# Kernel optimization log

Hardware: AMD Instinct MI355X
Metric: run time of the kernel (lower is better)

The kernel has to match this reference:

```python
import jax, jax.numpy as jnp
import numpy as np

EPS = 1e-5

def _layernorm(h):
    # parameter-free LayerNorm over last dim (elementwise_affine=False)
    mu = jnp.mean(h, axis=-1, keepdims=True)
    var = jnp.mean(jnp.square(h - mu), axis=-1, keepdims=True)
    return (h - mu) / jnp.sqrt(var + EPS)

def setup_inputs() -> dict:
    key = jax.random.key(0)
    k1, k2, k3, k4 = jax.random.split(key, 4)
    B, D, F_, I = 16, 37, 4096, 64
    x = jax.random.normal(k1, (B, D, F_), dtype=jnp.float32)
    s = 1.0 / np.sqrt(D)  # ~ torch Linear default init scale
    Wq = jax.random.normal(k2, (D, I), dtype=jnp.float32) * s
    Wk = jax.random.normal(k3, (D, I), dtype=jnp.float32) * s
    Wv = jax.random.normal(k4, (D, I), dtype=jnp.float32) * s
    return {"x": x, "Wq": Wq, "Wk": Wk, "Wv": Wv}

def reference(x, Wq, Wk, Wv):
    # x: [B, depth, featuresize] -> entities [B, F, depth]
    xb = jnp.transpose(x, (0, 2, 1))
    q = _layernorm(jnp.einsum('bfd,di->bfi', xb, Wq))
    k = _layernorm(jnp.einsum('bfd,di->bfi', xb, Wk))
    v = _layernorm(jnp.einsum('bfd,di->bfi', xb, Wv))
    d = q.shape[-1]
    att = jnp.einsum('bqi,bki->bqk', q, k) / jnp.sqrt(jnp.float32(d))
    # faithful to torch: softmax over dim=1 (the query axis), not the key axis
    weights = jax.nn.softmax(att, axis=-2)
    return jnp.einsum('bqk,bki->bqi', weights, v)
```

## Files before the change

### kernel.cpp

```cpp
#include <hip/hip_runtime.h>
#include <math.h>

#define B_  16
#define D_  37
#define F_  4096
#define I_  64
#define EPS 1e-5f
#define QSCALE 0.18033688011112042f
#define NQS 2

typedef unsigned short u16;
typedef __bf16 bf16x8 __attribute__((ext_vector_type(8)));
typedef __bf16 bf16x2v __attribute__((ext_vector_type(2)));
typedef float  f32x16 __attribute__((ext_vector_type(16)));
typedef float  f32x2v __attribute__((ext_vector_type(2)));
typedef unsigned int u32x4 __attribute__((ext_vector_type(4)));
typedef int i32x2 __attribute__((ext_vector_type(2)));

#define ZERO16 {0,0,0,0, 0,0,0,0, 0,0,0,0, 0,0,0,0}
#define MFMA32(a, b, c) __builtin_amdgcn_mfma_f32_32x32x16_bf16((a), (b), (c), 0, 0, 0)

#if __has_builtin(__builtin_amdgcn_exp2f)
#define EX2(x) __builtin_amdgcn_exp2f(x)
#else
#define EX2(x) exp2f(x)
#endif
#if __has_builtin(__builtin_amdgcn_rcpf)
#define RCP(x) __builtin_amdgcn_rcpf(x)
#else
#define RCP(x) (1.f / (x))
#endif

__device__ __forceinline__ u16 f2b(float f) {
  unsigned u = __builtin_bit_cast(unsigned, f);
  return (u16)((u + 0x7fffu + ((u >> 16) & 1u)) >> 16);
}
__device__ __forceinline__ unsigned pk2(float lo, float hi) {
  f32x2v f = {lo, hi};
  bf16x2v h = __builtin_convertvector(f, bf16x2v);
  return __builtin_bit_cast(unsigned, h);
}

__device__ __forceinline__ void plswap(unsigned& a, unsigned& b) {
#if __has_builtin(__builtin_amdgcn_permlane32_swap)
  i32x2 r = __builtin_amdgcn_permlane32_swap((int)a, (int)b, false, false);
  a = (unsigned)r[0];
  b = (unsigned)r[1];
#else
  const int lh = (int)((threadIdx.x & 63) >> 5);
  unsigned pa = (unsigned)__shfl_xor((int)a, 32, 64);
  unsigned pb = (unsigned)__shfl_xor((int)b, 32, 64);
  unsigned na = lh ? pb : a;
  unsigned nb = lh ? b : pa;
  a = na;
  b = nb;
#endif
}

__device__ __forceinline__ void build_af(const f32x16& s, bf16x8& f0, bf16x8& f1) {
  float e[16];
#pragma unroll
  for (int r = 0; r < 16; ++r) e[r] = EX2(s[r]);
  unsigned a = pk2(e[0], e[1]),   bq = pk2(e[2], e[3]);
  unsigned c = pk2(e[4], e[5]),   d  = pk2(e[6], e[7]);
  plswap(a, c);
  plswap(bq, d);
  u32x4 v0 = {a, bq, c, d};
  f0 = __builtin_bit_cast(bf16x8, v0);
  unsigned ee = pk2(e[8], e[9]),  ff = pk2(e[10], e[11]);
  unsigned g  = pk2(e[12], e[13]), h = pk2(e[14], e[15]);
  plswap(ee, g);
  plswap(ff, h);
  u32x4 v1 = {ee, ff, g, h};
  f1 = __builtin_bit_cast(bf16x8, v1);
}

__device__ __forceinline__ bf16x8 ldfrag(const u16* base, int row, int kb) {
  return *(const bf16x8*)(base + (row << 6) + ((kb ^ (row & 7)) << 3));
}
__device__ __forceinline__ void stage16(u16* dst, const u16* src, int c, int spitch) {
  const int r = c >> 3, cb = c & 7;
  const int4 v = *(const int4*)(src + (size_t)r * spitch + (cb << 3));
  *(int4*)(dst + (r << 6) + ((cb ^ (r & 7)) << 3)) = v;
}
__device__ __forceinline__ int soff_l(int c) {
  const int r = c >> 3, cb = c & 7;
  return (r << 6) + ((cb ^ (r & 7)) << 3);
}
__device__ __forceinline__ int soff_g(int c, int spitch) {
  return (c >> 3) * spitch + ((c & 7) << 3);
}

__global__ __launch_bounds__(256) void qkv_ln_k(
    const float* __restrict__ x,
    const float* __restrict__ Wq, const float* __restrict__ Wk,
    const float* __restrict__ Wv,
    u16* __restrict__ qn, u16* __restrict__ kn, u16* __restrict__ vt) {
  __shared__ float sW[3 * D_ * I_];
  __shared__ float xs[D_ * 64];
  __shared__ __align__(16) u16 vtile[64 * 72];

  const int t = threadIdx.x;
  const int b = blockIdx.y;
  const int f0 = blockIdx.x * 64;

  for (int i = t; i < D_ * I_; i += 256) {
    sW[i]               = Wq[i];
    sW[D_ * I_ + i]     = Wk[i];
    sW[2 * D_ * I_ + i] = Wv[i];
  }
  const float* xb = x + (size_t)b * D_ * F_ + f0;
  for (int i = t; i < D_ * 64; i += 256)
    xs[i] = xb[(size_t)(i >> 6) * F_ + (i & 63)];
  __syncthreads();

  const int lane = t & 63, w = t >> 6;

  for (int it = 0; it < 16; ++it) {
    const int fl = w * 16 + it;
    float hq = 0.f, hk = 0.f, hv = 0.f;
#pragma unroll
    for (int d = 0; d < D_; ++d) {
      const float xv = xs[d * 64 + fl];
      hq = fmaf(xv, sW[d * 64 + lane], hq);
      hk = fmaf(xv, sW[D_ * I_ + d * 64 + lane], hk);
      hv = fmaf(xv, sW[2 * D_ * I_ + d * 64 + lane], hv);
    }
    auto lnorm = [&](float a) -> float {
      float s = a;
#pragma unroll
      for (int o = 32; o > 0; o >>= 1) s += __shfl_xor(s, o, 64);
      const float mu = s * (1.f / 64.f);
      const float d0 = a - mu;
      float v = d0 * d0;
#pragma unroll
      for (int o = 32; o > 0; o >>= 1) v += __shfl_xor(v, o, 64);
      return d0 * rsqrtf(v * (1.f / 64.f) + EPS);
    };
    const size_t fo = ((size_t)b * F_ + f0 + fl) * I_ + lane;
    qn[fo] = f2b(lnorm(hq) * QSCALE);
    kn[fo] = f2b(lnorm(hk));
    vtile[lane * 72 + fl] = f2b(lnorm(hv));
  }
  __syncthreads();
  for (int p = 0; p < 2; ++p) {
    const int c = p * 256 + t;
    const int r = c >> 3, off = (c & 7) * 8;
    const int4 v = *(const int4*)&vtile[r * 72 + off];
    *(int4*)(vt + ((size_t)b * I_ + r) * F_ + f0 + off) = v;
  }
}

__global__ __launch_bounds__(256, 2) void attn_stats_k(
    const u16* __restrict__ qn, const u16* __restrict__ kn,
    float* __restrict__ zp) {
  __shared__ __align__(16) u16 sm[16384];

  const int t = threadIdx.x, lane = t & 63, w = t >> 6;
  const int l31 = lane & 31, lh = lane >> 5;
  const int b = blockIdx.y, k0 = blockIdx.x * 256, qh = blockIdx.z;

  const u16* kb = kn + ((size_t)b * F_ + k0) * I_;
#pragma unroll
  for (int p = 0; p < 8; ++p) stage16(sm, kb, p * 256 + t, 64);
  __syncthreads();
  bf16x8 kf[2][4];
#pragma unroll
  for (int kb2 = 0; kb2 < 2; ++kb2)
#pragma unroll
    for (int ic = 0; ic < 4; ++ic)
      kf[kb2][ic] = ldfrag(sm + (w * 64 + kb2 * 32) * 64, l31, ic * 2 + lh);
  __syncthreads();

  int qoff_l[2], qoff_g[2];
#pragma unroll
  for (int p = 0; p < 2; ++p) {
    const int c = p * 256 + t;
    qoff_l[p] = soff_l(c);
    qoff_g[p] = soff_g(c, 64);
  }

  const u16* qsrc = qn + ((size_t)b * F_ + qh * (F_ / NQS)) * I_;
#pragma unroll
  for (int p = 0; p < 2; ++p)
    *(int4*)(sm + qoff_l[p]) = *(const int4*)(qsrc + qoff_g[p]);
  qsrc += 64 * I_;

  float Zc[2][2] = {{0.f, 0.f}, {0.f, 0.f}};
  const int NC = F_ / NQS / 64;

  for (int c = 0; c < NC; ++c) {
    const int cur = (c & 1) * 4096;
    __syncthreads();
    if (c + 1 < NC) {
      const int nxt = cur ^ 4096;
#pragma unroll
      for (int p = 0; p < 2; ++p)
        *(int4*)(sm + nxt + qoff_l[p]) = *(const int4*)(qsrc + qoff_g[p]);
      qsrc += 64 * I_;
    }

    f32x16 a00 = ZERO16, a01 = ZERO16, a10 = ZERO16, a11 = ZERO16;
#pragma unroll
    for (int ic = 0; ic < 4; ++ic) {
      const bf16x8 q0f = ldfrag(sm + cur, l31, ic * 2 + lh);
      const bf16x8 q1f = ldfrag(sm + cur + 32 * 64, l31, ic * 2 + lh);
      a00 = MFMA32(q0f, kf[0][ic], a00);
      a01 = MFMA32(q0f, kf[1][ic], a01);
      a10 = MFMA32(q1f, kf[0][ic], a10);
      a11 = MFMA32(q1f, kf[1][ic], a11);
    }
#pragma unroll
    for (int r = 0; r < 16; ++r) {
      Zc[0][0] += EX2(a00[r]);
      Zc[0][1] += EX2(a01[r]);
      Zc[1][0] += EX2(a10[r]);
      Zc[1][1] += EX2(a11[r]);
    }
  }

#pragma unroll
  for (int kb2 = 0; kb2 < 2; ++kb2) {
    float Zt = Zc[0][kb2] + Zc[1][kb2];
    Zt += __shfl_xor(Zt, 32, 64);
    if (lane < 32)
      zp[((size_t)qh * B_ + b) * F_ + k0 + w * 64 + kb2 * 32 + lane] = Zt;
  }
}

__global__ __launch_bounds__(256) void vscale_k(u16* __restrict__ vt,
                                                const float* __restrict__ zp) {
  const int b = blockIdx.y;
  const int off = (blockIdx.x * 256 + (int)threadIdx.x) * 8;
  const int k = off & (F_ - 1);
  u16* p = vt + (size_t)b * I_ * F_ + off;
  const float* z0 = zp + (size_t)b * F_ + k;
  const float* z1 = zp + (size_t)B_ * F_ + (size_t)b * F_ + k;
  int4 raw = *(const int4*)p;
  u16 es[8], os[8];
  *(int4*)es = raw;
#pragma unroll
  for (int j = 0; j < 8; ++j) {
    const float v = __builtin_bit_cast(float, (unsigned)es[j] << 16);
    const float rz = RCP(z0[j] + z1[j]);
    os[j] = f2b(v * rz);
  }
  *(int4*)p = *(int4*)os;
}

__global__ __launch_bounds__(128, 2) void attn_out_k(
    const u16* __restrict__ qn, const u16* __restrict__ kn,
    const u16* __restrict__ vt, float* __restrict__ out) {
  __shared__ __align__(16) u16 sm[16384];

  const int t = threadIdx.x, lane = t & 63, w = t >> 6;
  const int l31 = lane & 31, lh = lane >> 5;
  const int b = blockIdx.y, q0 = blockIdx.x * 128;

  const u16* qb = qn + ((size_t)b * F_ + q0) * I_;
#pragma unroll
  for (int p = 0; p < 8; ++p) stage16(sm, qb, p * 128 + t, 64);
  __syncthreads();
  bf16x8 qf[2][4];
#pragma unroll
  for (int qb2 = 0; qb2 < 2; ++qb2)
#pragma unroll
    for (int ic = 0; ic < 4; ++ic)
      qf[qb2][ic] = ldfrag(sm + (w * 64 + qb2 * 32) * 64, l31, ic * 2 + lh);
  __syncthreads();

  int off_l[4], kg[4], vg[4];
#pragma unroll
  for (int p = 0; p < 4; ++p) {
    const int c = p * 128 + t;
    off_l[p] = soff_l(c);
    kg[p] = soff_g(c, 64);
    vg[p] = soff_g(c, F_);
  }

  const u16* ksrc = kn + (size_t)b * F_ * I_;
  const u16* vsrc = vt + (size_t)b * I_ * F_;
#pragma unroll
  for (int p = 0; p < 4; ++p) {
    *(int4*)(sm + off_l[p])        = *(const int4*)(ksrc + kg[p]);
    *(int4*)(sm + 8192 + off_l[p]) = *(const int4*)(vsrc + vg[p]);
  }
  ksrc += 64 * I_;
  vsrc += 64;

  f32x16 o00 = ZERO16, o01 = ZERO16, o10 = ZERO16, o11 = ZERO16;
  const int NC = F_ / 64;

  for (int c = 0; c < NC; ++c) {
    const int cur = (c & 1) * 4096;
    __syncthreads();
    if (c + 1 < NC) {
      const int nxt = cur ^ 4096;
#pragma unroll
      for (int p = 0; p < 4; ++p) {
        *(int4*)(sm + nxt + off_l[p])        = *(const int4*)(ksrc + kg[p]);
        *(int4*)(sm + 8192 + nxt + off_l[p]) = *(const int4*)(vsrc + vg[p]);
      }
      ksrc += 64 * I_;
      vsrc += 64;
    }

    const u16* Kc = sm + cur;
    f32x16 s00 = ZERO16, s01 = ZERO16, s10 = ZERO16, s11 = ZERO16;
#pragma unroll
    for (int ic = 0; ic < 4; ++ic) {
      const bf16x8 ak0 = ldfrag(Kc, l31, ic * 2 + lh);
      const bf16x8 ak1 = ldfrag(Kc + 32 * 64, l31, ic * 2 + lh);
      s00 = MFMA32(ak0, qf[0][ic], s00);
      s01 = MFMA32(ak0, qf[1][ic], s01);
      s10 = MFMA32(ak1, qf[0][ic], s10);
      s11 = MFMA32(ak1, qf[1][ic], s11);
    }

    bf16x8 af[2][4];
    build_af(s00, af[0][0], af[0][1]);
    build_af(s10, af[0][2], af[0][3]);
    build_af(s01, af[1][0], af[1][1]);
    build_af(s11, af[1][2], af[1][3]);

    const u16* Vc = sm + 8192 + cur;
#pragma unroll
    for (int kb4 = 0; kb4 < 4; ++kb4) {
      const bf16x8 bv0 = ldfrag(Vc, l31, kb4 * 2 + lh);
      const bf16x8 bv1 = ldfrag(Vc + 32 * 64, l31, kb4 * 2 + lh);
      o00 = MFMA32(af[0][kb4], bv0, o00);
      o01 = MFMA32(af[0][kb4], bv1, o01);
      o10 = MFMA32(af[1][kb4], bv0, o10);
      o11 = MFMA32(af[1][kb4], bv1, o11);
    }
  }

  float* ob = out + ((size_t)b * F_ + q0 + w * 64) * I_;
#pragma unroll
  for (int r = 0; r < 16; ++r) {
    const int qr = (r & 3) + 8 * (r >> 2) + 4 * lh;
    ob[(size_t)qr * I_ + l31]              = o00[r];
    ob[(size_t)qr * I_ + 32 + l31]         = o01[r];
    ob[(size_t)(32 + qr) * I_ + l31]       = o10[r];
    ob[(size_t)(32 + qr) * I_ + 32 + l31]  = o11[r];
  }
}

extern "C" void kernel_launch(void* const* d_in, const int* in_sizes, int n_in,
                              void* d_out, int out_size, void* d_ws,
                              size_t ws_size, hipStream_t stream) {
  const float* x  = (const float*)d_in[0];
  const float* Wq = (const float*)d_in[1];
  const float* Wk = (const float*)d_in[2];
  const float* Wv = (const float*)d_in[3];
  float* out = (float*)d_out;

  const size_t NBF = (size_t)B_ * F_ * I_;
  u16* qn   = (u16*)d_ws;
  u16* kn   = qn + NBF;
  u16* vt   = kn + NBF;
  float* zp = (float*)(vt + NBF);

  qkv_ln_k<<<dim3(F_ / 64, B_), 256, 0, stream>>>(x, Wq, Wk, Wv, qn, kn, vt);
  attn_stats_k<<<dim3(F_ / 256, B_, NQS), 256, 0, stream>>>(qn, kn, zp);
  vscale_k<<<dim3(I_ * F_ / 2048, B_), 256, 0, stream>>>(vt, zp);
  attn_out_k<<<dim3(F_ / 128, B_), 128, 0, stream>>>(qn, kn, vt, out);
}
```

Baseline: 273.5 us.

## Split attention output over key chunks with atomics and register-block QKV projection

The output kernel now splits the key axis four ways across a new grid dimension. Each block processes 32-key chunks with half the shared memory, and partial outputs are accumulated into the zeroed result with atomicAdd. The stats kernel doubles its query split and raises its occupancy hint, and vscale sums all partial Z values. The QKV projection drops its shared-memory staging and keeps 16 rows per wave in registers, reading x and weights directly from global memory. The extra parallelism and occupancy are meant to fill the GPU better, at the cost of atomic contention, an extra memset and a smaller MFMA tile per chunk.

```diff
diff --git a/kernel.cpp b/kernel.cpp
--- a/kernel.cpp
+++ b/kernel.cpp
@@ -7,7 +7,8 @@
 #define I_  64
 #define EPS 1e-5f
 #define QSCALE 0.18033688011112042f
-#define NQS 2
+#define NQS 4
+#define KSP 4
 
 typedef unsigned short u16;
 typedef __bf16 bf16x8 __attribute__((ext_vector_type(8)));
@@ -34,6 +35,9 @@
 __device__ __forceinline__ u16 f2b(float f) {
   unsigned u = __builtin_bit_cast(unsigned, f);
   return (u16)((u + 0x7fffu + ((u >> 16) & 1u)) >> 16);
+}
+__device__ __forceinline__ float b2f(u16 h) {
+  return __builtin_bit_cast(float, (unsigned)h << 16);
 }
 __device__ __forceinline__ unsigned pk2(float lo, float hi) {
   f32x2v f = {lo, hi};
@@ -78,6 +82,9 @@
 __device__ __forceinline__ bf16x8 ldfrag(const u16* base, int row, int kb) {
   return *(const bf16x8*)(base + (row << 6) + ((kb ^ (row & 7)) << 3));
 }
+__device__ __forceinline__ bf16x8 ldfrag32(const u16* base, int row, int kb) {
+  return *(const bf16x8*)(base + (row << 5) + ((kb ^ (row & 3)) << 3));
+}
 __device__ __forceinline__ void stage16(u16* dst, const u16* src, int c, int spitch) {
   const int r = c >> 3, cb = c & 7;
   const int4 v = *(const int4*)(src + (size_t)r * spitch + (cb << 3));
@@ -96,51 +103,52 @@
     const float* __restrict__ Wq, const float* __restrict__ Wk,
     const float* __restrict__ Wv,
     u16* __restrict__ qn, u16* __restrict__ kn, u16* __restrict__ vt) {
-  __shared__ float sW[3 * D_ * I_];
-  __shared__ float xs[D_ * 64];
   __shared__ __align__(16) u16 vtile[64 * 72];
 
-  const int t = threadIdx.x;
-  const int b = blockIdx.y;
-  const int f0 = blockIdx.x * 64;
-
-  for (int i = t; i < D_ * I_; i += 256) {
-    sW[i]               = Wq[i];
-    sW[D_ * I_ + i]     = Wk[i];
-    sW[2 * D_ * I_ + i] = Wv[i];
-  }
-  const float* xb = x + (size_t)b * D_ * F_ + f0;
-  for (int i = t; i < D_ * 64; i += 256)
-    xs[i] = xb[(size_t)(i >> 6) * F_ + (i & 63)];
-  __syncthreads();
-
-  const int lane = t & 63, w = t >> 6;
-
-  for (int it = 0; it < 16; ++it) {
-    const int fl = w * 16 + it;
-    float hq = 0.f, hk = 0.f, hv = 0.f;
-#pragma unroll
-    for (int d = 0; d < D_; ++d) {
-      const float xv = xs[d * 64 + fl];
-      hq = fmaf(xv, sW[d * 64 + lane], hq);
-      hk = fmaf(xv, sW[D_ * I_ + d * 64 + lane], hk);
-      hv = fmaf(xv, sW[2 * D_ * I_ + d * 64 + lane], hv);
-    }
-    auto lnorm = [&](float a) -> float {
-      float s = a;
-#pragma unroll
-      for (int o = 32; o > 0; o >>= 1) s += __shfl_xor(s, o, 64);
-      const float mu = s * (1.f / 64.f);
-      const float d0 = a - mu;
-      float v = d0 * d0;
-#pragma unroll
-      for (int o = 32; o > 0; o >>= 1) v += __shfl_xor(v, o, 64);
-      return d0 * rsqrtf(v * (1.f / 64.f) + EPS);
-    };
-    const size_t fo = ((size_t)b * F_ + f0 + fl) * I_ + lane;
-    qn[fo] = f2b(lnorm(hq) * QSCALE);
-    kn[fo] = f2b(lnorm(hk));
-    vtile[lane * 72 + fl] = f2b(lnorm(hv));
+  const int t = threadIdx.x, lane = t & 63, w = t >> 6;
+  const int b = blockIdx.y, f0 = blockIdx.x * 64;
+  const int fl0 = w * 16;
+
+  float hq[16], hk[16], hv[16];
+#pragma unroll
+  for (int i = 0; i < 16; ++i) { hq[i] = 0.f; hk[i] = 0.f; hv[i] = 0.f; }
+
+  const float* xb = x + (size_t)b * D_ * F_ + f0 + fl0;
+#pragma unroll 1
+  for (int d = 0; d < D_; ++d) {
+    const float wqv = Wq[d * I_ + lane];
+    const float wkv = Wk[d * I_ + lane];
+    const float wvv = Wv[d * I_ + lane];
+    float xv[16];
+#pragma unroll
+    for (int g = 0; g < 4; ++g)
+      *(float4*)&xv[g * 4] = *(const float4*)(xb + (size_t)d * F_ + g * 4);
+#pragma unroll
+    for (int i = 0; i < 16; ++i) {
+      hq[i] = fmaf(xv[i], wqv, hq[i]);
+      hk[i] = fmaf(xv[i], wkv, hk[i]);
+      hv[i] = fmaf(xv[i], wvv, hv[i]);
+    }
+  }
+
+  auto lnorm = [&](float a) -> float {
+    float s = a;
+#pragma unroll
+    for (int o = 32; o > 0; o >>= 1) s += __shfl_xor(s, o, 64);
+    const float mu = s * (1.f / 64.f);
+    const float d0 = a - mu;
+    float v = d0 * d0;
+#pragma unroll
+    for (int o = 32; o > 0; o >>= 1) v += __shfl_xor(v, o, 64);
+    return d0 * rsqrtf(v * (1.f / 64.f) + EPS);
+  };
+
+#pragma unroll
+  for (int i = 0; i < 16; ++i) {
+    const size_t fo = ((size_t)b * F_ + f0 + fl0 + i) * I_ + lane;
+    qn[fo] = f2b(lnorm(hq[i]) * QSCALE);
+    kn[fo] = f2b(lnorm(hk[i]));
+    vtile[lane * 72 + fl0 + i] = f2b(lnorm(hv[i]));
   }
   __syncthreads();
   for (int p = 0; p < 2; ++p) {
@@ -151,7 +159,7 @@
   }
 }
 
-__global__ __launch_bounds__(256, 2) void attn_stats_k(
+__global__ __launch_bounds__(256, 4) void attn_stats_k(
     const u16* __restrict__ qn, const u16* __restrict__ kn,
     float* __restrict__ zp) {
   __shared__ __align__(16) u16 sm[16384];
@@ -235,27 +243,27 @@
   const int k = off & (F_ - 1);
   u16* p = vt + (size_t)b * I_ * F_ + off;
   const float* z0 = zp + (size_t)b * F_ + k;
-  const float* z1 = zp + (size_t)B_ * F_ + (size_t)b * F_ + k;
   int4 raw = *(const int4*)p;
   u16 es[8], os[8];
   *(int4*)es = raw;
 #pragma unroll
   for (int j = 0; j < 8; ++j) {
-    const float v = __builtin_bit_cast(float, (unsigned)es[j] << 16);
-    const float rz = RCP(z0[j] + z1[j]);
-    os[j] = f2b(v * rz);
+    float z = z0[j];
+#pragma unroll
+    for (int pl = 1; pl < NQS; ++pl) z += z0[(size_t)pl * B_ * F_ + j];
+    os[j] = f2b(b2f(es[j]) * RCP(z));
   }
   *(int4*)p = *(int4*)os;
 }
 
-__global__ __launch_bounds__(128, 2) void attn_out_k(
+__global__ __launch_bounds__(128, 4) void attn_out_k(
     const u16* __restrict__ qn, const u16* __restrict__ kn,
     const u16* __restrict__ vt, float* __restrict__ out) {
-  __shared__ __align__(16) u16 sm[16384];
+  __shared__ __align__(16) u16 sm[8192];
 
   const int t = threadIdx.x, lane = t & 63, w = t >> 6;
   const int l31 = lane & 31, lh = lane >> 5;
-  const int b = blockIdx.y, q0 = blockIdx.x * 128;
+  const int b = blockIdx.y, q0 = blockIdx.x * 128, ks = blockIdx.z;
 
   const u16* qb = qn + ((size_t)b * F_ + q0) * I_;
 #pragma unroll
@@ -269,69 +277,66 @@
       qf[qb2][ic] = ldfrag(sm + (w * 64 + qb2 * 32) * 64, l31, ic * 2 + lh);
   __syncthreads();
 
-  int off_l[4], kg[4], vg[4];
-#pragma unroll
-  for (int p = 0; p < 4; ++p) {
+  int koff_l[2], koff_g[2], voff_l[2], voff_g[2];
+#pragma unroll
+  for (int p = 0; p < 2; ++p) {
     const int c = p * 128 + t;
-    off_l[p] = soff_l(c);
-    kg[p] = soff_g(c, 64);
-    vg[p] = soff_g(c, F_);
-  }
-
-  const u16* ksrc = kn + (size_t)b * F_ * I_;
-  const u16* vsrc = vt + (size_t)b * I_ * F_;
-#pragma unroll
-  for (int p = 0; p < 4; ++p) {
-    *(int4*)(sm + off_l[p])        = *(const int4*)(ksrc + kg[p]);
-    *(int4*)(sm + 8192 + off_l[p]) = *(const int4*)(vsrc + vg[p]);
-  }
-  ksrc += 64 * I_;
-  vsrc += 64;
+    koff_l[p] = soff_l(c);
+    koff_g[p] = soff_g(c, 64);
+    const int vr = c >> 2, vc = c & 3;
+    voff_l[p] = (vr << 5) + (((vc ^ (vr & 3))) << 3);
+    voff_g[p] = vr * F_ + (vc << 3);
+  }
+
+  const u16* ksrc = kn + ((size_t)b * F_ + ks * (F_ / KSP)) * I_;
+  const u16* vsrc = vt + (size_t)b * I_ * F_ + ks * (F_ / KSP);
+#pragma unroll
+  for (int p = 0; p < 2; ++p) {
+    *(int4*)(sm + koff_l[p])        = *(const int4*)(ksrc + koff_g[p]);
+    *(int4*)(sm + 4096 + voff_l[p]) = *(const int4*)(vsrc + voff_g[p]);
+  }
+  ksrc += 32 * I_;
+  vsrc += 32;
 
   f32x16 o00 = ZERO16, o01 = ZERO16, o10 = ZERO16, o11 = ZERO16;
-  const int NC = F_ / 64;
+  const int NC = F_ / KSP / 32;
 
   for (int c = 0; c < NC; ++c) {
-    const int cur = (c & 1) * 4096;
+    const int cur = (c & 1) * 2048;
     __syncthreads();
     if (c + 1 < NC) {
-      const int nxt = cur ^ 4096;
-#pragma unroll
-      for (int p = 0; p < 4; ++p) {
-        *(int4*)(sm + nxt + off_l[p])        = *(const int4*)(ksrc + kg[p]);
-        *(int4*)(sm + 8192 + nxt + off_l[p]) = *(const int4*)(vsrc + vg[p]);
+      const int nxt = cur ^ 2048;
+#pragma unroll
+      for (int p = 0; p < 2; ++p) {
+        *(int4*)(sm + nxt + koff_l[p])        = *(const int4*)(ksrc + koff_g[p]);
+        *(int4*)(sm + 4096 + nxt + voff_l[p]) = *(const int4*)(vsrc + voff_g[p]);
       }
-      ksrc += 64 * I_;
-      vsrc += 64;
+      ksrc += 32 * I_;
+      vsrc += 32;
     }
 
     const u16* Kc = sm + cur;
-    f32x16 s00 = ZERO16, s01 = ZERO16, s10 = ZERO16, s11 = ZERO16;
+    f32x16 s0 = ZERO16, s1 = ZERO16;
 #pragma unroll
     for (int ic = 0; ic < 4; ++ic) {
-      const bf16x8 ak0 = ldfrag(Kc, l31, ic * 2 + lh);
-      const bf16x8 ak1 = ldfrag(Kc + 32 * 64, l31, ic * 2 + lh);
-      s00 = MFMA32(ak0, qf[0][ic], s00);
-      s01 = MFMA32(ak0, qf[1][ic], s01);
-      s10 = MFMA32(ak1, qf[0][ic], s10);
-      s11 = MFMA32(ak1, qf[1][ic], s11);
-    }
-
-    bf16x8 af[2][4];
-    build_af(s00, af[0][0], af[0][1]);
-    build_af(s10, af[0][2], af[0][3]);
-    build_af(s01, af[1][0], af[1][1]);
-    build_af(s11, af[1][2], af[1][3]);
-
-    const u16* Vc = sm + 8192 + cur;
-#pragma unroll
-    for (int kb4 = 0; kb4 < 4; ++kb4) {
-      const bf16x8 bv0 = ldfrag(Vc, l31, kb4 * 2 + lh);
-      const bf16x8 bv1 = ldfrag(Vc + 32 * 64, l31, kb4 * 2 + lh);
-      o00 = MFMA32(af[0][kb4], bv0, o00);
-      o01 = MFMA32(af[0][kb4], bv1, o01);
-      o10 = MFMA32(af[1][kb4], bv0, o10);
-      o11 = MFMA32(af[1][kb4], bv1, o11);
+      const bf16x8 ak = ldfrag(Kc, l31, ic * 2 + lh);
+      s0 = MFMA32(ak, qf[0][ic], s0);
+      s1 = MFMA32(ak, qf[1][ic], s1);
+    }
+
+    bf16x8 af0[2], af1[2];
+    build_af(s0, af0[0], af0[1]);
+    build_af(s1, af1[0], af1[1]);
+
+    const u16* Vc = sm + 4096 + cur;
+#pragma unroll
+    for (int kb2 = 0; kb2 < 2; ++kb2) {
+      const bf16x8 bv0 = ldfrag32(Vc, l31, kb2 * 2 + lh);
+      const bf16x8 bv1 = ldfrag32(Vc + 32 * 32, l31, kb2 * 2 + lh);
+      o00 = MFMA32(af0[kb2], bv0, o00);
+      o01 = MFMA32(af0[kb2], bv1, o01);
+      o10 = MFMA32(af1[kb2], bv0, o10);
+      o11 = MFMA32(af1[kb2], bv1, o11);
     }
   }
 
@@ -339,10 +344,10 @@
 #pragma unroll
   for (int r = 0; r < 16; ++r) {
     const int qr = (r & 3) + 8 * (r >> 2) + 4 * lh;
-    ob[(size_t)qr * I_ + l31]              = o00[r];
-    ob[(size_t)qr * I_ + 32 + l31]         = o01[r];
-    ob[(size_t)(32 + qr) * I_ + l31]       = o10[r];
-    ob[(size_t)(32 + qr) * I_ + 32 + l31]  = o11[r];
+    atomicAdd(&ob[(size_t)qr * I_ + l31],             o00[r]);
+    atomicAdd(&ob[(size_t)qr * I_ + 32 + l31],        o01[r]);
+    atomicAdd(&ob[(size_t)(32 + qr) * I_ + l31],      o10[r]);
+    atomicAdd(&ob[(size_t)(32 + qr) * I_ + 32 + l31], o11[r]);
   }
 }
 
@@ -361,8 +366,9 @@
   u16* vt   = kn + NBF;
   float* zp = (float*)(vt + NBF);
 
+  hipMemsetAsync(out, 0, (size_t)out_size * sizeof(float), stream);
   qkv_ln_k<<<dim3(F_ / 64, B_), 256, 0, stream>>>(x, Wq, Wk, Wv, qn, kn, vt);
   attn_stats_k<<<dim3(F_ / 256, B_, NQS), 256, 0, stream>>>(qn, kn, zp);
   vscale_k<<<dim3(I_ * F_ / 2048, B_), 256, 0, stream>>>(vt, zp);
-  attn_out_k<<<dim3(F_ / 128, B_), 128, 0, stream>>>(qn, kn, vt, out);
-}
+  attn_out_k<<<dim3(F_ / 128, B_, KSP), 128, 0, stream>>>(qn, kn, vt, out);
+}
```

New measurement: 384.2 us. 40.5% more time.
